# Performance work log

Measured on AMD Instinct MI355X. Metric: run time of the kernel, lower is better.

The kernel has to match this reference:

```python
import jax, jax.numpy as jnp
import numpy as np

U = 100_000   # user_cnt
I = 200_000   # item_cnt
D = 128       # embed_dim
E = 3_200_000 # interactions (symmetric nnz = 2*E)
B = 16_384    # batch of (user, item) pairs


def setup_inputs() -> dict:
    key = jax.random.key(0)
    k1, k2, k3, k4, k5, k6, k7 = jax.random.split(key, 7)
    user_emb = jax.random.normal(k1, (U, D), dtype=jnp.float32) * 0.1
    item_emb = jax.random.normal(k2, (I, D), dtype=jnp.float32) * 0.1
    # bipartite symmetric adjacency: user->item edges and their transposes
    rows_u = jax.random.randint(k3, (E,), 0, U, dtype=jnp.int32)
    cols_i = jax.random.randint(k4, (E,), U, U + I, dtype=jnp.int32)
    adj_rows = jnp.concatenate([rows_u, cols_i])
    adj_cols = jnp.concatenate([cols_i, rows_u])
    vals_half = jax.random.uniform(k5, (E,), dtype=jnp.float32, minval=0.01, maxval=0.2)
    adj_vals = jnp.concatenate([vals_half, vals_half])  # symmetric normalized weights
    user_indices = jax.random.randint(k6, (B,), 0, U, dtype=jnp.int32)
    item_indices = jax.random.randint(k7, (B,), 0, I, dtype=jnp.int32)
    return {"user_emb": user_emb, "item_emb": item_emb, "adj_vals": adj_vals,
            "adj_rows": adj_rows, "adj_cols": adj_cols,
            "user_indices": user_indices, "item_indices": item_indices}


def reference(user_emb, item_emb, adj_vals, adj_rows, adj_cols, user_indices, item_indices):
    N = U + I
    # layer-0 embedding: concat users then items, as in torch.cat
    e0 = jnp.concatenate([user_emb, item_emb], axis=0)            # [N, D]
    # one sparse propagation: e1 = A @ e0 via gather -> scale -> segment_sum
    e1 = jax.ops.segment_sum(adj_vals[:, None] * e0[adj_cols], adj_rows,
                             num_segments=N)                       # [N, D]
    final = (e0 + e1) * 0.5                                        # mean over 2 layers
    u = final[:U][user_indices]                                    # [B, D]
    it = final[U:][item_indices]                                   # [B, D]
    return jnp.sum(u * it, axis=1)                                 # [B]
```

## Files before the change

### kernel.cpp

```cpp
#include <hip/hip_runtime.h>

#define EMB_D 128
#define SLOT_CAP 96

__global__ void claim_kernel(const int* __restrict__ user_idx,
                             const int* __restrict__ item_idx,
                             int* __restrict__ node_map, int B, int U) {
    int t = blockIdx.x * blockDim.x + threadIdx.x;
    if (t >= 2 * B) return;
    int node = (t < B) ? user_idx[t] : (U + item_idx[t - B]);
    atomicCAS(&node_map[node], 0, t + 1);
}

__global__ void fill_kernel(const float* __restrict__ user_emb,
                            const float* __restrict__ item_emb,
                            const float* __restrict__ vals,
                            const int* __restrict__ rows,
                            const int* __restrict__ cols,
                            const int* __restrict__ node_map,
                            int* __restrict__ deg,
                            int2* __restrict__ edge_buf,
                            float* __restrict__ comp,
                            int nnz, int U) {
    int e = blockIdx.x * blockDim.x + threadIdx.x;
    if (e >= nnz) return;
    int s = node_map[rows[e]];
    if (s == 0) return;
    int slot = s - 1;
    int pos = atomicAdd(&deg[slot], 1);
    int c = cols[e];
    float v = vals[e];
    if (pos < SLOT_CAP) {
        edge_buf[(size_t)slot * SLOT_CAP + pos] = make_int2(c, __float_as_int(v));
    } else {
        const float* src = (c < U) ? (user_emb + (size_t)c * EMB_D)
                                   : (item_emb + (size_t)(c - U) * EMB_D);
        float* dst = comp + (size_t)slot * EMB_D;
        for (int i = 0; i < EMB_D; ++i) atomicAdd(dst + i, v * src[i]);
    }
}

__global__ void gather_kernel(const float* __restrict__ user_emb,
                              const float* __restrict__ item_emb,
                              const int2* __restrict__ edge_buf,
                              const int* __restrict__ deg,
                              float* __restrict__ comp,
                              int nslots, int U) {
    int wid  = (blockIdx.x * blockDim.x + threadIdx.x) >> 6;
    int lane = threadIdx.x & 63;
    if (wid >= nslots) return;
    int d = deg[wid];
    if (d == 0) return;
    if (d > SLOT_CAP) d = SLOT_CAP;
    const int2* eb = edge_buf + (size_t)wid * SLOT_CAP;
    float2 acc = make_float2(0.f, 0.f);
    for (int j = 0; j < d; ++j) {
        int2 ed = eb[j];
        int   c = ed.x;
        float v = __int_as_float(ed.y);
        const float* src = (c < U) ? (user_emb + (size_t)c * EMB_D)
                                   : (item_emb + (size_t)(c - U) * EMB_D);
        float2 x = *(const float2*)(src + lane * 2);
        acc.x = fmaf(v, x.x, acc.x);
        acc.y = fmaf(v, x.y, acc.y);
    }
    float* dst = comp + (size_t)wid * EMB_D + lane * 2;
    dst[0] += acc.x;
    dst[1] += acc.y;
}

__global__ void final_kernel(const float* __restrict__ user_emb,
                             const float* __restrict__ item_emb,
                             const int* __restrict__ user_idx,
                             const int* __restrict__ item_idx,
                             const int* __restrict__ node_map,
                             const float* __restrict__ comp,
                             float* __restrict__ out, int B, int U) {
    int wid  = (blockIdx.x * blockDim.x + threadIdx.x) >> 6;
    int lane = threadIdx.x & 63;
    if (wid >= B) return;
    int un  = user_idx[wid];
    int inn = item_idx[wid];
    int su  = node_map[un] - 1;
    int si  = node_map[U + inn] - 1;
    float2 eu = *(const float2*)(user_emb + (size_t)un * EMB_D + lane * 2);
    float2 ei = *(const float2*)(item_emb + (size_t)inn * EMB_D + lane * 2);
    float2 cu = *(const float2*)(comp + (size_t)su * EMB_D + lane * 2);
    float2 ci = *(const float2*)(comp + (size_t)si * EMB_D + lane * 2);
    float p = (eu.x + cu.x) * (ei.x + ci.x) + (eu.y + cu.y) * (ei.y + ci.y);
#pragma unroll
    for (int off = 32; off; off >>= 1) p += __shfl_down(p, off);
    if (lane == 0) out[wid] = 0.25f * p;
}

__global__ void scatter_kernel(const float* __restrict__ user_emb,
                               const float* __restrict__ item_emb,
                               const float* __restrict__ vals,
                               const int* __restrict__ rows,
                               const int* __restrict__ cols,
                               const int* __restrict__ node_map,
                               float* __restrict__ comp,
                               int nnz, int U) {
    int e = blockIdx.x * blockDim.x + threadIdx.x;
    int lane = threadIdx.x & 63;
    int s = 0; int c = 0; float v = 0.f;
    if (e < nnz) {
        int r = rows[e];
        s = node_map[r];
        if (s != 0) { c = cols[e]; v = vals[e]; }
    }
    unsigned long long mask = __ballot(s != 0);
    while (mask) {
        int j = __ffsll(mask) - 1;
        mask &= mask - 1;
        int   cj    = __shfl(c, j);
        float vj    = __shfl(v, j);
        int   slotj = __shfl(s, j) - 1;
        const float* src = (cj < U) ? (user_emb + (size_t)cj * EMB_D)
                                    : (item_emb + (size_t)(cj - U) * EMB_D);
        float2 x = *(const float2*)(src + lane * 2);
        float* dst = comp + (size_t)slotj * EMB_D + lane * 2;
        atomicAdd(dst,     x.x * vj);
        atomicAdd(dst + 1, x.y * vj);
    }
}

extern "C" void kernel_launch(void* const* d_in, const int* in_sizes, int n_in,
                              void* d_out, int out_size, void* d_ws, size_t ws_size,
                              hipStream_t stream) {
    const float* user_emb = (const float*)d_in[0];
    const float* item_emb = (const float*)d_in[1];
    const float* adj_vals = (const float*)d_in[2];
    const int*   adj_rows = (const int*)d_in[3];
    const int*   adj_cols = (const int*)d_in[4];
    const int*   user_idx = (const int*)d_in[5];
    const int*   item_idx = (const int*)d_in[6];
    float* out = (float*)d_out;

    int U   = in_sizes[0] / EMB_D;
    int I   = in_sizes[1] / EMB_D;
    int N   = U + I;
    int nnz = in_sizes[2];
    int B   = in_sizes[5];
    int S   = 2 * B;

    size_t comp_bytes = (size_t)S * EMB_D * sizeof(float);
    size_t map_bytes  = ((size_t)N * sizeof(int) + 15) & ~(size_t)15;
    size_t deg_bytes  = (size_t)S * sizeof(int);
    size_t edge_bytes = (size_t)S * SLOT_CAP * sizeof(int2);

    float* comp     = (float*)d_ws;
    int*   node_map = (int*)((char*)d_ws + comp_bytes);
    int*   deg      = (int*)((char*)d_ws + comp_bytes + map_bytes);
    int2*  edge_buf = (int2*)((char*)d_ws + comp_bytes + map_bytes + deg_bytes);

    if (ws_size >= comp_bytes + map_bytes + deg_bytes + edge_bytes) {
        hipMemsetAsync(d_ws, 0, comp_bytes + map_bytes + deg_bytes, stream);
        claim_kernel<<<(S + 255) / 256, 256, 0, stream>>>(user_idx, item_idx,
                                                          node_map, B, U);
        fill_kernel<<<(nnz + 255) / 256, 256, 0, stream>>>(user_emb, item_emb,
                                                           adj_vals, adj_rows,
                                                           adj_cols, node_map,
                                                           deg, edge_buf, comp,
                                                           nnz, U);
        gather_kernel<<<(S * 64 + 255) / 256, 256, 0, stream>>>(user_emb, item_emb,
                                                                edge_buf, deg, comp,
                                                                S, U);
    } else {
        hipMemsetAsync(d_ws, 0, comp_bytes + map_bytes, stream);
        claim_kernel<<<(S + 255) / 256, 256, 0, stream>>>(user_idx, item_idx,
                                                          node_map, B, U);
        scatter_kernel<<<(nnz + 255) / 256, 256, 0, stream>>>(user_emb, item_emb,
                                                              adj_vals, adj_rows,
                                                              adj_cols, node_map,
                                                              comp, nnz, U);
    }
    final_kernel<<<(B * 64 + 255) / 256, 256, 0, stream>>>(user_emb, item_emb,
                                                           user_idx, item_idx,
                                                           node_map, comp, out,
                                                           B, U);
}
```

Measured before the change: 162.5 us.

## Vectorize fill row loads and batch gather edge loads with wave shuffles

The fill kernel now processes four edges per thread, reading rows with an int4 load and issuing four node_map lookups together before the per-edge atomics. The gather kernel loads up to 64 edge entries at once, one per lane, then broadcasts each neighbor pointer and weight by shuffle. It issues eight independent row loads per iteration into separate accumulators, which raises memory-level parallelism over the old serial dependent chain. Non-overflow slots are written directly instead of read-modify-written, at the cost of more registers and padded dummy loads in the last batch.

```diff
diff --git a/kernel.cpp b/kernel.cpp
--- a/kernel.cpp
+++ b/kernel.cpp
@@ -12,19 +12,11 @@
     atomicCAS(&node_map[node], 0, t + 1);
 }
 
-__global__ void fill_kernel(const float* __restrict__ user_emb,
-                            const float* __restrict__ item_emb,
-                            const float* __restrict__ vals,
-                            const int* __restrict__ rows,
-                            const int* __restrict__ cols,
-                            const int* __restrict__ node_map,
-                            int* __restrict__ deg,
-                            int2* __restrict__ edge_buf,
-                            float* __restrict__ comp,
-                            int nnz, int U) {
-    int e = blockIdx.x * blockDim.x + threadIdx.x;
-    if (e >= nnz) return;
-    int s = node_map[rows[e]];
+__device__ __forceinline__ void fill_one(int e, int s,
+        const float* __restrict__ user_emb, const float* __restrict__ item_emb,
+        const float* __restrict__ vals, const int* __restrict__ cols,
+        int* __restrict__ deg, int2* __restrict__ edge_buf,
+        float* __restrict__ comp, int U) {
     if (s == 0) return;
     int slot = s - 1;
     int pos = atomicAdd(&deg[slot], 1);
@@ -40,6 +32,36 @@
     }
 }
 
+__global__ void fill_kernel(const float* __restrict__ user_emb,
+                            const float* __restrict__ item_emb,
+                            const float* __restrict__ vals,
+                            const int* __restrict__ rows,
+                            const int* __restrict__ cols,
+                            const int* __restrict__ node_map,
+                            int* __restrict__ deg,
+                            int2* __restrict__ edge_buf,
+                            float* __restrict__ comp,
+                            int nnz, int U) {
+    int t = blockIdx.x * blockDim.x + threadIdx.x;
+    int e = t * 4;
+    if (e >= nnz) return;
+    if (e + 3 < nnz) {
+        int4 r4 = *(const int4*)(rows + e);
+        int s0 = node_map[r4.x];
+        int s1 = node_map[r4.y];
+        int s2 = node_map[r4.z];
+        int s3 = node_map[r4.w];
+        fill_one(e,     s0, user_emb, item_emb, vals, cols, deg, edge_buf, comp, U);
+        fill_one(e + 1, s1, user_emb, item_emb, vals, cols, deg, edge_buf, comp, U);
+        fill_one(e + 2, s2, user_emb, item_emb, vals, cols, deg, edge_buf, comp, U);
+        fill_one(e + 3, s3, user_emb, item_emb, vals, cols, deg, edge_buf, comp, U);
+    } else {
+        for (int k = e; k < nnz; ++k)
+            fill_one(k, node_map[rows[k]], user_emb, item_emb, vals, cols,
+                     deg, edge_buf, comp, U);
+    }
+}
+
 __global__ void gather_kernel(const float* __restrict__ user_emb,
                               const float* __restrict__ item_emb,
                               const int2* __restrict__ edge_buf,
@@ -50,23 +72,66 @@
     int lane = threadIdx.x & 63;
     if (wid >= nslots) return;
     int d = deg[wid];
-    if (d == 0) return;
-    if (d > SLOT_CAP) d = SLOT_CAP;
+    bool ovf = (d > SLOT_CAP);
+    int dc = ovf ? SLOT_CAP : d;
     const int2* eb = edge_buf + (size_t)wid * SLOT_CAP;
-    float2 acc = make_float2(0.f, 0.f);
-    for (int j = 0; j < d; ++j) {
+    float* dst = comp + (size_t)wid * EMB_D + lane * 2;
+
+    int2 my_e = eb[lane];
+    int  myc  = my_e.x;
+    const float* mybase = (myc < U) ? (user_emb + (size_t)myc * EMB_D)
+                                    : (item_emb + (size_t)(myc - U) * EMB_D);
+    unsigned long long mba = (unsigned long long)mybase;
+    int   b_lo = (int)(unsigned)mba;
+    int   b_hi = (int)(mba >> 32);
+    float myv  = __int_as_float(my_e.y);
+
+    float2 a[8];
+#pragma unroll
+    for (int k = 0; k < 8; ++k) a[k] = make_float2(0.f, 0.f);
+
+    int n0 = dc < 64 ? dc : 64;
+    for (int j = 0; j < n0; j += 8) {
+        const float* p[8];
+        float vv[8];
+#pragma unroll
+        for (int k = 0; k < 8; ++k) {
+            int jj = (j + k < n0) ? (j + k) : (n0 - 1);
+            int   lo = __shfl(b_lo, jj);
+            int   hi = __shfl(b_hi, jj);
+            float v  = __shfl(myv, jj);
+            vv[k] = (j + k < n0) ? v : 0.f;
+            p[k]  = (const float*)(((unsigned long long)(unsigned)hi << 32)
+                                   | (unsigned)lo);
+        }
+        float2 x[8];
+#pragma unroll
+        for (int k = 0; k < 8; ++k) x[k] = *(const float2*)(p[k] + lane * 2);
+#pragma unroll
+        for (int k = 0; k < 8; ++k) {
+            a[k].x = fmaf(vv[k], x[k].x, a[k].x);
+            a[k].y = fmaf(vv[k], x[k].y, a[k].y);
+        }
+    }
+
+    float2 tl = make_float2(0.f, 0.f);
+    for (int j = 64; j < dc; ++j) {
         int2 ed = eb[j];
-        int   c = ed.x;
+        int c = ed.x;
         float v = __int_as_float(ed.y);
         const float* src = (c < U) ? (user_emb + (size_t)c * EMB_D)
                                    : (item_emb + (size_t)(c - U) * EMB_D);
         float2 x = *(const float2*)(src + lane * 2);
-        acc.x = fmaf(v, x.x, acc.x);
-        acc.y = fmaf(v, x.y, acc.y);
-    }
-    float* dst = comp + (size_t)wid * EMB_D + lane * 2;
-    dst[0] += acc.x;
-    dst[1] += acc.y;
+        tl.x = fmaf(v, x.x, tl.x);
+        tl.y = fmaf(v, x.y, tl.y);
+    }
+
+    float rx = ((a[0].x + a[1].x) + (a[2].x + a[3].x))
+             + ((a[4].x + a[5].x) + (a[6].x + a[7].x)) + tl.x;
+    float ry = ((a[0].y + a[1].y) + (a[2].y + a[3].y))
+             + ((a[4].y + a[5].y) + (a[6].y + a[7].y)) + tl.y;
+    if (ovf) { dst[0] += rx; dst[1] += ry; }
+    else     { dst[0] = rx;  dst[1] = ry; }
 }
 
 __global__ void final_kernel(const float* __restrict__ user_emb,
@@ -158,11 +223,10 @@
         hipMemsetAsync(d_ws, 0, comp_bytes + map_bytes + deg_bytes, stream);
         claim_kernel<<<(S + 255) / 256, 256, 0, stream>>>(user_idx, item_idx,
                                                           node_map, B, U);
-        fill_kernel<<<(nnz + 255) / 256, 256, 0, stream>>>(user_emb, item_emb,
-                                                           adj_vals, adj_rows,
-                                                           adj_cols, node_map,
-                                                           deg, edge_buf, comp,
-                                                           nnz, U);
+        int fill_threads = (nnz + 3) / 4;
+        fill_kernel<<<(fill_threads + 255) / 256, 256, 0, stream>>>(
+            user_emb, item_emb, adj_vals, adj_rows, adj_cols, node_map,
+            deg, edge_buf, comp, nnz, U);
         gather_kernel<<<(S * 64 + 255) / 256, 256, 0, stream>>>(user_emb, item_emb,
                                                                 edge_buf, deg, comp,
                                                                 S, U);
```

New measurement: 139.1 us. -14.4%, faster.

## Batch fill edges per block with ILP loads; widen gather to float4 with unrolled edges

Applied to the files above, without the earlier changes.

The fill kernel now has each block process 2048 edges, issuing eight independent row loads and eight node_map lookups per thread before compacting the matching edges into shared memory, then doing the global degree atomics. The gather kernel loads the first 64 edge entries into the wavefront once, broadcasts pointers and weights via shuffles, and has each half-wave read float4s for eight edges per iteration with separate accumulators, then combines the halves. Both aim to raise memory-level parallelism and cut dependent-load latency. The cost is more registers and shared memory, plus extra shuffle work.

```diff
diff --git a/kernel.cpp b/kernel.cpp
--- a/kernel.cpp
+++ b/kernel.cpp
@@ -2,6 +2,8 @@
 
 #define EMB_D 128
 #define SLOT_CAP 96
+#define FILL_CHUNK 2048
+#define FILL_THREADS 256
 
 __global__ void claim_kernel(const int* __restrict__ user_idx,
                              const int* __restrict__ item_idx,
@@ -12,61 +14,171 @@
     atomicCAS(&node_map[node], 0, t + 1);
 }
 
-__global__ void fill_kernel(const float* __restrict__ user_emb,
-                            const float* __restrict__ item_emb,
-                            const float* __restrict__ vals,
-                            const int* __restrict__ rows,
-                            const int* __restrict__ cols,
-                            const int* __restrict__ node_map,
-                            int* __restrict__ deg,
-                            int2* __restrict__ edge_buf,
-                            float* __restrict__ comp,
-                            int nnz, int U) {
-    int e = blockIdx.x * blockDim.x + threadIdx.x;
-    if (e >= nnz) return;
-    int s = node_map[rows[e]];
-    if (s == 0) return;
-    int slot = s - 1;
-    int pos = atomicAdd(&deg[slot], 1);
-    int c = cols[e];
-    float v = vals[e];
-    if (pos < SLOT_CAP) {
-        edge_buf[(size_t)slot * SLOT_CAP + pos] = make_int2(c, __float_as_int(v));
-    } else {
-        const float* src = (c < U) ? (user_emb + (size_t)c * EMB_D)
-                                   : (item_emb + (size_t)(c - U) * EMB_D);
-        float* dst = comp + (size_t)slot * EMB_D;
-        for (int i = 0; i < EMB_D; ++i) atomicAdd(dst + i, v * src[i]);
-    }
-}
-
-__global__ void gather_kernel(const float* __restrict__ user_emb,
-                              const float* __restrict__ item_emb,
-                              const int2* __restrict__ edge_buf,
-                              const int* __restrict__ deg,
-                              float* __restrict__ comp,
-                              int nslots, int U) {
+__device__ __forceinline__ void slow_place_cv(int slot, int c, float v,
+        float* __restrict__ comp,
+        const float* __restrict__ user_emb, const float* __restrict__ item_emb,
+        int U) {
+    const float* src = (c < U) ? (user_emb + (size_t)c * EMB_D)
+                               : (item_emb + (size_t)(c - U) * EMB_D);
+    float* dst = comp + (size_t)slot * EMB_D;
+    for (int i = 0; i < EMB_D; ++i) atomicAdd(dst + i, v * src[i]);
+}
+
+__global__ void __launch_bounds__(FILL_THREADS)
+fill2_kernel(const float* __restrict__ user_emb,
+             const float* __restrict__ item_emb,
+             const float* __restrict__ vals,
+             const int* __restrict__ rows,
+             const int* __restrict__ cols,
+             const int* __restrict__ node_map,
+             int* __restrict__ deg,
+             int2* __restrict__ edge_buf,
+             float* __restrict__ comp,
+             int nnz, int U) {
+    __shared__ int  l_slot[FILL_CHUNK];
+    __shared__ int2 l_cv[FILL_CHUNK];
+    __shared__ int  lcount;
+    const int tid = threadIdx.x;
+    if (tid == 0) lcount = 0;
+    __syncthreads();
+
+    const long long base = (long long)blockIdx.x * FILL_CHUNK;
+    const int K = FILL_CHUNK / FILL_THREADS;
+    int r8[K];
+    int s8[K];
+#pragma unroll
+    for (int k = 0; k < K; ++k) {
+        long long e = base + (long long)k * FILL_THREADS + tid;
+        r8[k] = (e < nnz) ? rows[e] : -1;
+    }
+#pragma unroll
+    for (int k = 0; k < K; ++k)
+        s8[k] = (r8[k] >= 0) ? node_map[r8[k]] : 0;
+#pragma unroll
+    for (int k = 0; k < K; ++k) {
+        if (s8[k] != 0) {
+            long long e = base + (long long)k * FILL_THREADS + tid;
+            int p = atomicAdd(&lcount, 1);
+            l_slot[p] = s8[k] - 1;
+            l_cv[p]   = make_int2(cols[e], __float_as_int(vals[e]));
+        }
+    }
+    __syncthreads();
+
+    int n = lcount;
+    for (int i = tid; i < n; i += FILL_THREADS) {
+        int  slot = l_slot[i];
+        int2 cv   = l_cv[i];
+        int pos = atomicAdd(&deg[slot], 1);
+        if (pos < SLOT_CAP)
+            edge_buf[(size_t)slot * SLOT_CAP + pos] = cv;
+        else
+            slow_place_cv(slot, cv.x, __int_as_float(cv.y),
+                          comp, user_emb, item_emb, U);
+    }
+}
+
+__device__ __forceinline__ void gk_fetch(int j, int k, int h, int n0,
+                                         int b_lo, int b_hi, float myv,
+                                         const float*& pk, float& vk) {
+    int jj  = j + 2 * k + h;
+    int src = (jj < n0) ? jj : (n0 - 1);
+    int lo = __shfl(b_lo, src);
+    int hi = __shfl(b_hi, src);
+    float vx = __shfl(myv, src);
+    vk = (jj < n0) ? vx : 0.f;
+    pk = (const float*)((((unsigned long long)(unsigned)hi) << 32)
+                        | (unsigned)lo);
+}
+
+__device__ __forceinline__ void fma4(float4& acc, float v, const float4& val) {
+    acc.x = fmaf(v, val.x, acc.x);
+    acc.y = fmaf(v, val.y, acc.y);
+    acc.z = fmaf(v, val.z, acc.z);
+    acc.w = fmaf(v, val.w, acc.w);
+}
+
+__global__ void __launch_bounds__(256, 1)
+gather_kernel(const float* __restrict__ user_emb,
+              const float* __restrict__ item_emb,
+              const int2* __restrict__ edge_buf,
+              const int* __restrict__ deg,
+              float* __restrict__ comp,
+              int nslots, int U) {
     int wid  = (blockIdx.x * blockDim.x + threadIdx.x) >> 6;
     int lane = threadIdx.x & 63;
     if (wid >= nslots) return;
     int d = deg[wid];
-    if (d == 0) return;
-    if (d > SLOT_CAP) d = SLOT_CAP;
+    bool ovf = (d > SLOT_CAP);
+    int dc = ovf ? SLOT_CAP : d;
     const int2* eb = edge_buf + (size_t)wid * SLOT_CAP;
-    float2 acc = make_float2(0.f, 0.f);
-    for (int j = 0; j < d; ++j) {
+    const int h = lane >> 5;
+    const int q = lane & 31;
+
+    int2 my_e = eb[lane];
+    int  myc  = my_e.x;
+    const float* mybase = (myc < U) ? (user_emb + (size_t)myc * EMB_D)
+                                    : (item_emb + (size_t)(myc - U) * EMB_D);
+    unsigned long long mba = (unsigned long long)mybase;
+    int   b_lo = (int)(unsigned)mba;
+    int   b_hi = (int)(mba >> 32);
+    float myv  = __int_as_float(my_e.y);
+
+    float4 a0 = {0,0,0,0}, a1 = {0,0,0,0}, a2 = {0,0,0,0}, a3 = {0,0,0,0};
+    float4 a4 = {0,0,0,0}, a5 = {0,0,0,0}, a6 = {0,0,0,0}, a7 = {0,0,0,0};
+
+    const int n0 = dc < 64 ? dc : 64;
+    for (int j = 0; j < n0; j += 16) {
+        const float *p0, *p1, *p2, *p3, *p4, *p5, *p6, *p7;
+        float v0, v1, v2, v3, v4, v5, v6, v7;
+        gk_fetch(j, 0, h, n0, b_lo, b_hi, myv, p0, v0);
+        gk_fetch(j, 1, h, n0, b_lo, b_hi, myv, p1, v1);
+        gk_fetch(j, 2, h, n0, b_lo, b_hi, myv, p2, v2);
+        gk_fetch(j, 3, h, n0, b_lo, b_hi, myv, p3, v3);
+        gk_fetch(j, 4, h, n0, b_lo, b_hi, myv, p4, v4);
+        gk_fetch(j, 5, h, n0, b_lo, b_hi, myv, p5, v5);
+        gk_fetch(j, 6, h, n0, b_lo, b_hi, myv, p6, v6);
+        gk_fetch(j, 7, h, n0, b_lo, b_hi, myv, p7, v7);
+        float4 x0 = *(const float4*)(p0 + q * 4);
+        float4 x1 = *(const float4*)(p1 + q * 4);
+        float4 x2 = *(const float4*)(p2 + q * 4);
+        float4 x3 = *(const float4*)(p3 + q * 4);
+        float4 x4 = *(const float4*)(p4 + q * 4);
+        float4 x5 = *(const float4*)(p5 + q * 4);
+        float4 x6 = *(const float4*)(p6 + q * 4);
+        float4 x7 = *(const float4*)(p7 + q * 4);
+        fma4(a0, v0, x0); fma4(a1, v1, x1); fma4(a2, v2, x2); fma4(a3, v3, x3);
+        fma4(a4, v4, x4); fma4(a5, v5, x5); fma4(a6, v6, x6); fma4(a7, v7, x7);
+    }
+
+    float4 r;
+    r.x = ((a0.x + a1.x) + (a2.x + a3.x)) + ((a4.x + a5.x) + (a6.x + a7.x));
+    r.y = ((a0.y + a1.y) + (a2.y + a3.y)) + ((a4.y + a5.y) + (a6.y + a7.y));
+    r.z = ((a0.z + a1.z) + (a2.z + a3.z)) + ((a4.z + a5.z) + (a6.z + a7.z));
+    r.w = ((a0.w + a1.w) + (a2.w + a3.w)) + ((a4.w + a5.w) + (a6.w + a7.w));
+    r.x += __shfl_xor(r.x, 32);
+    r.y += __shfl_xor(r.y, 32);
+    r.z += __shfl_xor(r.z, 32);
+    r.w += __shfl_xor(r.w, 32);
+
+    for (int j = 64; j < dc; ++j) {
         int2 ed = eb[j];
-        int   c = ed.x;
+        int c = ed.x;
         float v = __int_as_float(ed.y);
         const float* src = (c < U) ? (user_emb + (size_t)c * EMB_D)
                                    : (item_emb + (size_t)(c - U) * EMB_D);
-        float2 x = *(const float2*)(src + lane * 2);
-        acc.x = fmaf(v, x.x, acc.x);
-        acc.y = fmaf(v, x.y, acc.y);
-    }
-    float* dst = comp + (size_t)wid * EMB_D + lane * 2;
-    dst[0] += acc.x;
-    dst[1] += acc.y;
+        float4 xx = *(const float4*)(src + q * 4);
+        fma4(r, v, xx);
+    }
+
+    if (h == 0) {
+        float4* dst = (float4*)(comp + (size_t)wid * EMB_D) + q;
+        if (ovf) {
+            float4 o = *dst;
+            r.x += o.x; r.y += o.y; r.z += o.z; r.w += o.w;
+        }
+        *dst = r;
+    }
 }
 
 __global__ void final_kernel(const float* __restrict__ user_emb,
@@ -111,17 +223,17 @@
     }
     unsigned long long mask = __ballot(s != 0);
     while (mask) {
-        int j = __ffsll(mask) - 1;
+        int j = __ffsll((long long)mask) - 1;
         mask &= mask - 1;
         int   cj    = __shfl(c, j);
         float vj    = __shfl(v, j);
         int   slotj = __shfl(s, j) - 1;
         const float* src = (cj < U) ? (user_emb + (size_t)cj * EMB_D)
                                     : (item_emb + (size_t)(cj - U) * EMB_D);
-        float2 x = *(const float2*)(src + lane * 2);
+        float2 xx = *(const float2*)(src + lane * 2);
         float* dst = comp + (size_t)slotj * EMB_D + lane * 2;
-        atomicAdd(dst,     x.x * vj);
-        atomicAdd(dst + 1, x.y * vj);
+        atomicAdd(dst,     xx.x * vj);
+        atomicAdd(dst + 1, xx.y * vj);
     }
 }
 
@@ -146,23 +258,23 @@
 
     size_t comp_bytes = (size_t)S * EMB_D * sizeof(float);
     size_t map_bytes  = ((size_t)N * sizeof(int) + 15) & ~(size_t)15;
-    size_t deg_bytes  = (size_t)S * sizeof(int);
+    size_t deg_bytes  = (((size_t)S) * sizeof(int) + 15) & ~(size_t)15;
     size_t edge_bytes = (size_t)S * SLOT_CAP * sizeof(int2);
+    size_t fixed      = comp_bytes + map_bytes + deg_bytes + edge_bytes;
 
     float* comp     = (float*)d_ws;
     int*   node_map = (int*)((char*)d_ws + comp_bytes);
     int*   deg      = (int*)((char*)d_ws + comp_bytes + map_bytes);
     int2*  edge_buf = (int2*)((char*)d_ws + comp_bytes + map_bytes + deg_bytes);
 
-    if (ws_size >= comp_bytes + map_bytes + deg_bytes + edge_bytes) {
+    if (ws_size >= fixed) {
         hipMemsetAsync(d_ws, 0, comp_bytes + map_bytes + deg_bytes, stream);
         claim_kernel<<<(S + 255) / 256, 256, 0, stream>>>(user_idx, item_idx,
                                                           node_map, B, U);
-        fill_kernel<<<(nnz + 255) / 256, 256, 0, stream>>>(user_emb, item_emb,
-                                                           adj_vals, adj_rows,
-                                                           adj_cols, node_map,
-                                                           deg, edge_buf, comp,
-                                                           nnz, U);
+        int fill_blocks = (int)((nnz + FILL_CHUNK - 1) / FILL_CHUNK);
+        fill2_kernel<<<fill_blocks, FILL_THREADS, 0, stream>>>(
+            user_emb, item_emb, adj_vals, adj_rows, adj_cols, node_map,
+            deg, edge_buf, comp, nnz, U);
         gather_kernel<<<(S * 64 + 255) / 256, 256, 0, stream>>>(user_emb, item_emb,
                                                                 edge_buf, deg, comp,
                                                                 S, U);
```

After: 145.1 us. -10.7%, faster.
